# Performance work log

Hardware: AMD Instinct MI355X
Metric: run time of the kernel (lower is better)

The kernel has to match this reference:

```python
import jax, jax.numpy as jnp
import numpy as np
import math

N = 20000          # real nodes (batch_size)
D = 256            # hidden_dim
H = 4              # num_heads
L = 3              # num_layers
E = 320000         # local edges
EXP_DEG = 4        # expander_degree
LN_EPS = 1e-5


def setup_inputs() -> dict:
    key = jax.random.key(0)
    ks = jax.random.split(key, 8)
    x = jax.random.normal(ks[0], (N, D), jnp.float32)
    rng = np.random.default_rng(0)
    edge_index = jnp.asarray(rng.integers(0, N, size=(2, E)), dtype=jnp.int32)
    # Expander: EXP_DEG//2 random permutations on N+1 nodes (incl. virtual node),
    # each contributing edges in both directions -> degree-EXP_DEG regular graph.
    n = N + 1
    perms = [rng.permutation(n) for _ in range(EXP_DEG // 2)]
    src = np.concatenate([np.arange(n) for _ in perms] + perms)
    dst = np.concatenate(perms + [np.arange(n) for _ in perms])
    exp_edge_index = jnp.asarray(np.stack([src, dst]), dtype=jnp.int32)
    s_in = 1.0 / math.sqrt(D)
    s_ffn = 1.0 / math.sqrt(4 * D)
    def w(k, shape, s):
        return jax.random.normal(k, shape, jnp.float32) * s
    params = {
        'Wqkv_loc': w(ks[1], (L, D, 3 * D), s_in), 'bqkv_loc': jnp.zeros((L, 3 * D), jnp.float32),
        'Wo_loc':   w(ks[2], (L, D, D), s_in),     'bo_loc':   jnp.zeros((L, D), jnp.float32),
        'Wqkv_exp': w(ks[3], (L, D, 3 * D), s_in), 'bqkv_exp': jnp.zeros((L, 3 * D), jnp.float32),
        'Wo_exp':   w(ks[4], (L, D, D), s_in),     'bo_exp':   jnp.zeros((L, D), jnp.float32),
        'ln_g': jnp.ones((L, D), jnp.float32),     'ln_b': jnp.zeros((L, D), jnp.float32),
        'W1': w(ks[5], (L, D, 4 * D), s_in),       'b1': jnp.zeros((L, 4 * D), jnp.float32),
        'W2': w(ks[6], (L, 4 * D, D), s_ffn),      'b2': jnp.zeros((L, D), jnp.float32),
    }
    return {'x': x, 'edge_index': edge_index, 'exp_edge_index': exp_edge_index, **params}


def _attention(h, src, dst, Wqkv, bqkv, Wo, bo):
    # Sparse multi-head attention over (src -> dst) edges with segment softmax per dst.
    n, d = h.shape
    dh = d // H
    qkv = (h @ Wqkv + bqkv).reshape(n, 3, H, dh)
    q, k, v = qkv[:, 0], qkv[:, 1], qkv[:, 2]            # [n, H, dh]
    score = (q[dst] * k[src]).sum(-1) / jnp.sqrt(jnp.float32(dh))  # [e, H]
    m = jax.ops.segment_max(score, dst, num_segments=n)  # [n, H]
    ex = jnp.exp(score - m[dst])
    denom = jax.ops.segment_sum(ex, dst, num_segments=n)
    alpha = ex / (denom[dst] + 1e-16)
    out = jax.ops.segment_sum(alpha[:, :, None] * v[src], dst, num_segments=n)  # [n, H, dh]
    return out.reshape(n, d) @ Wo + bo


def _layer_norm(x, g, b):
    mu = x.mean(-1, keepdims=True)
    var = ((x - mu) ** 2).mean(-1, keepdims=True)
    return (x - mu) * jax.lax.rsqrt(var + LN_EPS) * g + b


def reference(x, edge_index, exp_edge_index, Wqkv_loc, bqkv_loc, Wo_loc, bo_loc,
              Wqkv_exp, bqkv_exp, Wo_exp, bo_exp, ln_g, ln_b, W1, b1, W2, b2):
    n0 = x.shape[0]
    # VirtualNode transform: append one zero-feature node connected to/from all nodes.
    h = jnp.concatenate([x, jnp.zeros((1, x.shape[1]), x.dtype)], axis=0)
    ar = jnp.arange(n0, dtype=edge_index.dtype)
    vn = jnp.full((n0,), n0, dtype=edge_index.dtype)
    src = jnp.concatenate([edge_index[0], ar, vn])
    dst = jnp.concatenate([edge_index[1], vn, ar])
    esrc, edst = exp_edge_index[0], exp_edge_index[1]
    for l in range(L):  # fixed small number of structurally distinct layers
        res = h
        loc = _attention(h, src, dst, Wqkv_loc[l], bqkv_loc[l], Wo_loc[l], bo_loc[l])
        exp = _attention(h, esrc, edst, Wqkv_exp[l], bqkv_exp[l], Wo_exp[l], bo_exp[l])
        h = _layer_norm(res + loc + exp, ln_g[l], ln_b[l])
        h = h + (jax.nn.gelu(h @ W1[l] + b1[l], approximate=False) @ W2[l] + b2[l])
    return h[:n0]
```

## Files before the change

### kernel.cpp

```cpp
#include <hip/hip_runtime.h>
#include <stdint.h>

#define NREAL   20000
#define NNODES  20001
#define VN      20000
#define E_EDGES 320000
#define NEXP    80004
#define MPAD    20096
#define NVNW    320

typedef unsigned short u16;
typedef unsigned int   u32;
typedef __bf16 bf16x8 __attribute__((ext_vector_type(8)));
typedef float  f32x4  __attribute__((ext_vector_type(4)));
typedef u16    u16x8  __attribute__((ext_vector_type(8)));

__device__ __host__ __forceinline__ size_t fmoff(int row, int col, int LD) {
    return (size_t)(row >> 4) * ((size_t)LD * 16) + (size_t)((col >> 3) * 128)
         + (size_t)((row & 15) * 8) + (size_t)(col & 7);
}

__device__ __forceinline__ int qkv_perm(int n) {
    if (n < 256) return n;
    int u = n - 256;
    int part = u >> 8;
    int cl = u & 255;
    return 256 + (cl >> 2) * 8 + part * 4 + (cl & 3);
}

__device__ __forceinline__ float bf2f(u16 v) {
    union { u32 u; float f; } x; x.u = ((u32)v) << 16; return x.f;
}
__device__ __forceinline__ u16 f2bf(float f) {
    union { float f; u32 u; } x; x.f = f;
    u32 r = (x.u + 0x7fffu + ((x.u >> 16) & 1u)) >> 16;
    return (u16)r;
}
__device__ __forceinline__ float4 cvt4(ushort4 u) {
    return make_float4(bf2f(u.x), bf2f(u.y), bf2f(u.z), bf2f(u.w));
}
__device__ __forceinline__ float4 ld4bf(const u16* p) { return cvt4(*(const ushort4*)p); }
__device__ __forceinline__ float4 cvtk8(u16x8 r) {
    return make_float4(bf2f(r[0]), bf2f(r[1]), bf2f(r[2]), bf2f(r[3]));
}
__device__ __forceinline__ float4 cvtv8(u16x8 r) {
    return make_float4(bf2f(r[4]), bf2f(r[5]), bf2f(r[6]), bf2f(r[7]));
}


__global__ void hinit_kernel(const float* __restrict__ x, float* __restrict__ h,
                             u16* __restrict__ hb) {
    int idx = blockIdx.x * 256 + threadIdx.x;
    if (idx >= NNODES * 64) return;
    int row = idx >> 6, c0 = (idx & 63) * 4;
    float4 v = make_float4(0.f, 0.f, 0.f, 0.f);
    if (row < NREAL) v = *(const float4*)(x + (size_t)row * 256 + c0);
    *(float4*)(h + (size_t)row * 256 + c0) = v;
    ushort4 o;
    o.x = f2bf(v.x); o.y = f2bf(v.y); o.z = f2bf(v.z); o.w = f2bf(v.w);
    *(ushort4*)(hb + fmoff(row, c0, 256)) = o;
}

__global__ void init_kernel(int* cnt, int* fill, int* ecnt,
                            const float* __restrict__ bl, const float* __restrict__ be,
                            float* __restrict__ bcat,
                            const float* __restrict__ bol, const float* __restrict__ boe,
                            float* __restrict__ bsum) {
    int i = blockIdx.x * 256 + threadIdx.x;
    if (i < NREAL) { cnt[i] = 0; fill[i] = 0; }
    if (i < NNODES) ecnt[i] = 0;
    if (i < 3 * 1536) {
        int l = i / 1536, c = i - l * 1536;
        float v = (c < 768) ? bl[l * 768 + c] : be[l * 768 + c - 768];
        int cc = (c >= 768) ? c - 768 : c;
        int d = qkv_perm(cc) + ((c >= 768) ? 768 : 0);
        bcat[l * 1536 + d] = v;
    }
    if (i < 3 * 256) bsum[i] = bol[i] + boe[i];
}

__global__ void csr_count_kernel(const int* __restrict__ ei, int* __restrict__ cnt) {
    int e = blockIdx.x * 256 + threadIdx.x;
    if (e < E_EDGES) atomicAdd(&cnt[ei[E_EDGES + e]], 1);
}

__global__ void csr_scan_kernel(const int* __restrict__ cnt, int* __restrict__ indptr) {
    __shared__ int ssum[256];
    int t = threadIdx.x;
    int c0 = t * 79;
    int s = 0;
    for (int j = 0; j < 79; j++) {
        int i = c0 + j;
        if (i < NREAL) s += cnt[i];
    }
    ssum[t] = s;
    __syncthreads();
    for (int d2 = 1; d2 < 256; d2 <<= 1) {
        int v = (t >= d2) ? ssum[t - d2] : 0;
        __syncthreads();
        ssum[t] += v;
        __syncthreads();
    }
    int run = (t == 0) ? 0 : ssum[t - 1];
    for (int j = 0; j < 79; j++) {
        int i = c0 + j;
        if (i < NREAL) { indptr[i] = run; run += cnt[i]; }
    }
    if (t == 255) indptr[NREAL] = run;
}

__global__ void csr_scatter_kernel(const int* __restrict__ ei, const int* __restrict__ indptr,
                                   int* __restrict__ fill, int* __restrict__ srcs) {
    int e = blockIdx.x * 256 + threadIdx.x;
    if (e < E_EDGES) {
        int d = ei[E_EDGES + e];
        int pos = indptr[d] + atomicAdd(&fill[d], 1);
        srcs[pos] = ei[e];
    }
}

__global__ void exp_scatter_kernel(const int* __restrict__ eei, int* __restrict__ ecnt,
                                   int* __restrict__ esrcs) {
    int e = blockIdx.x * 256 + threadIdx.x;
    if (e < NEXP) {
        int d = eei[NEXP + e];
        int pos = atomicAdd(&ecnt[d], 1);
        esrcs[d * 4 + pos] = eei[e];
    }
}

__global__ void wconv_all_kernel(const float* __restrict__ WqkvL, const float* __restrict__ WqkvE,
                                 const float* __restrict__ WoL, const float* __restrict__ WoE,
                                 const float* __restrict__ W1, const float* __restrict__ W2,
                                 u16* __restrict__ out) {
    int i = blockIdx.x * 256 + threadIdx.x;
    if (i >= 3 * 1048576) return;
    int l = i / 1048576, r = i - l * 1048576;
    if (r >= 393216 && r < 524288) {
        int r2 = r - 393216;
        int k = r2 >> 8, n = r2 & 255;
        float v = (k < 256) ? WoL[(size_t)l * 65536 + k * 256 + n]
                            : WoE[(size_t)l * 65536 + (k - 256) * 256 + n];
        out[(size_t)l * 1048576 + 393216 + fmoff(n, k, 512)] = f2bf(v);
        return;
    }
    const float* src; int K, N; int base;
    if (r < 196608)      { src = WqkvL; K = 256;  N = 768;  base = 0; }
    else if (r < 393216) { src = WqkvE; K = 256;  N = 768;  base = 196608; }
    else if (r < 786432) { src = W1;    K = 256;  N = 1024; base = 524288; }
    else                 { src = W2;    K = 1024; N = 256;  base = 786432; }
    int r2 = r - base;
    int k = r2 / N, n = r2 - k * N;
    int d = (r < 393216) ? qkv_perm(n) : n;
    out[(size_t)l * 1048576 + base + fmoff(d, k, K)] = f2bf(src[(size_t)l * K * N + r2]);
}

template <int EPI>
__global__ __launch_bounds__(256) void gemm_bn(
    const u16* __restrict__ A, const u16* __restrict__ Bt, const float* __restrict__ bias,
    u16* Cb, u16* Q0, u16* KV0, u16* Q1, u16* KV1, int M, int Nout, int nbn) {
    __shared__ u16 lB[128 * 256];
    const int lin = blockIdx.x;
    const int xcd = lin & 7, rest = lin >> 3;
    const int nt = rest % nbn, mc = xcd + 8 * (rest / nbn);
    const int tn = nt * 128;
    const int tid = threadIdx.x;
    const int w = tid >> 6, lane = tid & 63;
    const int lm = lane & 15, q = lane >> 4;

    {
        const u16* bsrc = Bt + (size_t)(tn >> 4) * 4096;
#pragma unroll
        for (int r = 0; r < 16; r++) {
            int o = (r * 256 + tid) * 8;
            *(bf16x8*)&lB[o] = *(const bf16x8*)&bsrc[o];
        }
    }
    __syncthreads();

    f32x4 acc[2][8];
#pragma unroll
    for (int a = 0; a < 2; a++)
#pragma unroll
        for (int b = 0; b < 8; b++) acc[a][b] = (f32x4)0.0f;

    const int lbo = q * 128 + lm * 8;
    const int maxp = MPAD / 16 - 1;

    bf16x8 aS[3][2], bS[2][8];
#pragma unroll
    for (int s = 0; s < 2; s++) {
        int p0 = (mc * 4) * 8 + w * 2;
#pragma unroll
        for (int f = 0; f < 2; f++) {
            int p = p0 + f; if (p > maxp) p = maxp;
            aS[s][f] = *(const bf16x8*)(A + (size_t)p * 4096 + s * 512 + lbo);
        }
#pragma unroll
        for (int n = 0; n < 8; n++)
            bS[s][n] = *(const bf16x8*)&lB[n * 4096 + s * 512 + lbo];
    }

#pragma unroll
    for (int t = 0; t < 32; t++) {
        const int mt = t >> 3, kk = t & 7;
        if (t + 2 < 32) {
            const int t2 = t + 2, mt2 = t2 >> 3, kk2 = t2 & 7;
            int p0 = (mc * 4 + mt2) * 8 + w * 2;
#pragma unroll
            for (int f = 0; f < 2; f++) {
                int p = p0 + f; if (p > maxp) p = maxp;
                aS[t2 % 3][f] = *(const bf16x8*)(A + (size_t)p * 4096 + kk2 * 512 + lbo);
            }
        }
        if (t >= 1 && t + 1 < 32) {
            const int kk1 = (t + 1) & 7;
#pragma unroll
            for (int n = 0; n < 8; n++)
                bS[(t + 1) & 1][n] = *(const bf16x8*)&lB[n * 4096 + kk1 * 512 + lbo];
        }
#pragma unroll
        for (int mi = 0; mi < 2; mi++)
#pragma unroll
            for (int ni = 0; ni < 8; ni++)
                acc[mi][ni] = __builtin_amdgcn_mfma_f32_16x16x32_bf16(
                    bS[t & 1][ni], aS[t % 3][mi], acc[mi][ni], 0, 0, 0);

        if (kk == 7) {
            const int tmg = (mc * 4 + mt) * 128;
#pragma unroll
            for (int mi = 0; mi < 2; mi++) {
                int grow = tmg + w * 32 + mi * 16 + lm;
                if (grow < M) {
#pragma unroll
                    for (int ni = 0; ni < 8; ni++) {
                        int gcol = tn + ni * 16 + q * 4;
                        float4 b4 = *(const float4*)(bias + gcol);
                        float v0 = acc[mi][ni][0] + b4.x;
                        float v1 = acc[mi][ni][1] + b4.y;
                        float v2 = acc[mi][ni][2] + b4.z;
                        float v3 = acc[mi][ni][3] + b4.w;
                        if constexpr (EPI == 6) {
                            ushort4 o;
                            o.x = f2bf(v0); o.y = f2bf(v1); o.z = f2bf(v2); o.w = f2bf(v3);
                            u16* dst;
                            if (gcol < 256)       dst = Q0  + (size_t)grow * 256 + gcol;
                            else if (gcol < 768)  dst = KV0 + (size_t)grow * 512 + (gcol - 256);
                            else if (gcol < 1024) dst = Q1  + (size_t)grow * 256 + (gcol - 768);
                            else                  dst = KV1 + (size_t)grow * 512 + (gcol - 1024);
                            *(ushort4*)dst = o;
                        } else {
                            float g0, g1, g2, g3;
                            {
                                float u = 0.7978845608f * (v0 + 0.044715f * v0 * v0 * v0);
                                g0 = 0.5f * v0 * (2.0f - 2.0f / (__expf(2.0f * u) + 1.0f));
                            }
                            {
                                float u = 0.7978845608f * (v1 + 0.044715f * v1 * v1 * v1);
                                g1 = 0.5f * v1 * (2.0f - 2.0f / (__expf(2.0f * u) + 1.0f));
                            }
                            {
                                float u = 0.7978845608f * (v2 + 0.044715f * v2 * v2 * v2);
                                g2 = 0.5f * v2 * (2.0f - 2.0f / (__expf(2.0f * u) + 1.0f));
                            }
                            {
                                float u = 0.7978845608f * (v3 + 0.044715f * v3 * v3 * v3);
                                g3 = 0.5f * v3 * (2.0f - 2.0f / (__expf(2.0f * u) + 1.0f));
                            }
                            ushort4 o;
                            o.x = f2bf(g0); o.y = f2bf(g1); o.z = f2bf(g2); o.w = f2bf(g3);
                            *(ushort4*)(Cb + fmoff(grow, gcol, Nout)) = o;
                        }
                    }
                }
#pragma unroll
                for (int ni = 0; ni < 8; ni++) acc[mi][ni] = (f32x4)0.0f;
            }
        }
    }
}

template <int EPI, int K, int MT>
__global__ __launch_bounds__(256) void gemm_fm(
    const u16* __restrict__ A, const u16* __restrict__ Bt, const float* __restrict__ bias,
    u16* Cb, float* Cf, const float* resid, int M, int Nout, int nby) {
    constexpr int MFR = MT / 32;
    constexpr int NK = K / 32;
    const int lin = blockIdx.x;
    const int xcd = lin & 7, sub = lin >> 3;
    const int mtile = xcd + 8 * (sub / nby);
    const int ntile = sub - (sub / nby) * nby;
    const int tm = mtile * MT, tn = ntile * 128;
    if (tm >= M) return;

    const int tid = threadIdx.x;
    const int w = tid >> 6, lane = tid & 63;
    const int lm = lane & 15, q = lane >> 4;
    const int mo = (w >> 1) * (MT / 2), no = (w & 1) * 64;

    f32x4 acc[MFR][4];
#pragma unroll
    for (int a = 0; a < MFR; a++)
#pragma unroll
        for (int b = 0; b < 4; b++) acc[a][b] = (f32x4)0.0f;

    const u16* apf[MFR];
    const u16* bpf[4];
#pragma unroll
    for (int t = 0; t < MFR; t++) {
        int p = (tm + mo) / 16 + t;
        apf[t] = A + (size_t)p * (16 * K) + q * 128 + lm * 8;
    }
#pragma unroll
    for (int n = 0; n < 4; n++) {
        int c = (tn + no) / 16 + n;
        bpf[n] = Bt + (size_t)c * (16 * K) + q * 128 + lm * 8;
    }

    bf16x8 sA[3][MFR], sB[3][4];
#pragma unroll
    for (int s = 0; s < 2 && s < NK; s++) {
#pragma unroll
        for (int t = 0; t < MFR; t++) sA[s][t] = *(const bf16x8*)(apf[t] + s * 512);
#pragma unroll
        for (int n = 0; n < 4; n++) sB[s][n] = *(const bf16x8*)(bpf[n] + s * 512);
    }
#pragma unroll
    for (int i = 0; i < NK; i++) {
        const int cu = i % 3, pf = (i + 2) % 3;
        if (i + 2 < NK) {
#pragma unroll
            for (int t = 0; t < MFR; t++) sA[pf][t] = *(const bf16x8*)(apf[t] + (i + 2) * 512);
#pragma unroll
            for (int n = 0; n < 4; n++) sB[pf][n] = *(const bf16x8*)(bpf[n] + (i + 2) * 512);
        }
#pragma unroll
        for (int mi = 0; mi < MFR; mi++)
#pragma unroll
            for (int ni = 0; ni < 4; ni++)
                acc[mi][ni] = __builtin_amdgcn_mfma_f32_16x16x32_bf16(
                    sB[cu][ni], sA[cu][mi], acc[mi][ni], 0, 0, 0);
    }

    float4 b4[4];
#pragma unroll
    for (int ni = 0; ni < 4; ni++)
        b4[ni] = *(const float4*)(bias + tn + no + ni * 16 + q * 4);

#pragma unroll
    for (int mi = 0; mi < MFR; mi++) {
        int grow = tm + mo + mi * 16 + lm;
        if constexpr (EPI == 4) { if (grow >= NREAL) continue; }
        else                    { if (grow >= M) continue; }
#pragma unroll
        for (int ni = 0; ni < 4; ni++) {
            int gcol = tn + no + ni * 16 + q * 4;
            float v0 = acc[mi][ni][0] + b4[ni].x;
            float v1 = acc[mi][ni][1] + b4[ni].y;
            float v2 = acc[mi][ni][2] + b4[ni].z;
            float v3 = acc[mi][ni][3] + b4[ni].w;
            size_t idx = (size_t)grow * Nout + gcol;
            if constexpr (EPI == 1) {
                *(float4*)(Cf + idx) = make_float4(v0, v1, v2, v3);
            } else if constexpr (EPI == 3) {
                float4 rv = *(const float4*)(resid + idx);
                float o0 = rv.x + v0, o1 = rv.y + v1, o2 = rv.z + v2, o3 = rv.w + v3;
                *(float4*)(Cf + idx) = make_float4(o0, o1, o2, o3);
                ushort4 o;
                o.x = f2bf(o0); o.y = f2bf(o1); o.z = f2bf(o2); o.w = f2bf(o3);
                *(ushort4*)(Cb + fmoff(grow, gcol, Nout)) = o;
            } else {
                float4 rv = *(const float4*)(resid + idx);
                *(float4*)(Cf + idx) = make_float4(rv.x + v0, rv.y + v1, rv.z + v2, rv.w + v3);
            }
        }
    }
}

__global__ void vn_merge_kernel(const float* __restrict__ part, u16* __restrict__ acat) {
    __shared__ float sm[4][64][6];
    int w = threadIdx.x >> 6, lane = threadIdx.x & 63;
    int h = lane >> 4;
    int off = (h << 6) + (lane & 15) * 4;
    float M = -1e30f, L = 0.0f;
    float ax = 0, ay = 0, az = 0, aw = 0;
    for (int p = w * 80; p < w * 80 + 80; p++) {
        const float* pp = part + (size_t)p * 264;
        float pm = pp[h], pl = pp[4 + h];
        float4 nm = *(const float4*)(pp + 8 + off);
        float Mn = fmaxf(M, pm);
        float s0 = __expf(M - Mn);
        float s1 = __expf(pm - Mn);
        ax = ax * s0 + nm.x * s1;
        ay = ay * s0 + nm.y * s1;
        az = az * s0 + nm.z * s1;
        aw = aw * s0 + nm.w * s1;
        L = L * s0 + pl * s1;
        M = Mn;
    }
    sm[w][lane][0] = M; sm[w][lane][1] = L;
    sm[w][lane][2] = ax; sm[w][lane][3] = ay;
    sm[w][lane][4] = az; sm[w][lane][5] = aw;
    __syncthreads();
    if (w == 0) {
        float M2 = -1e30f, L2 = 0.0f;
        float bx = 0, by = 0, bz = 0, bw = 0;
#pragma unroll
        for (int p = 0; p < 4; p++) {
            float pm = sm[p][lane][0], pl = sm[p][lane][1];
            float Mn = fmaxf(M2, pm);
            float s0 = __expf(M2 - Mn);
            float s1 = __expf(pm - Mn);
            bx = bx * s0 + sm[p][lane][2] * s1;
            by = by * s0 + sm[p][lane][3] * s1;
            bz = bz * s0 + sm[p][lane][4] * s1;
            bw = bw * s0 + sm[p][lane][5] * s1;
            L2 = L2 * s0 + pl * s1;
            M2 = Mn;
        }
        float inv = 1.0f / (L2 + 1e-16f);
        ushort4 o;
        o.x = f2bf(bx * inv); o.y = f2bf(by * inv);
        o.z = f2bf(bz * inv); o.w = f2bf(bw * inv);
        *(ushort4*)(acat + fmoff(VN, off, 512)) = o;
    }
}

__global__ void attn_fused_kernel(const u16* __restrict__ qb_loc, const u16* __restrict__ kv_loc,
                                  const u16* __restrict__ qb_exp, const u16* __restrict__ kv_exp,
                                  const int* __restrict__ indptr, const int* __restrict__ srcs,
                                  const int* __restrict__ esrcs,
                                  u16* __restrict__ acat, float* __restrict__ part) {
    int gw0 = (int)((blockIdx.x * (size_t)blockDim.x + threadIdx.x) >> 6);
    int gw = __builtin_amdgcn_readfirstlane(gw0);
    int lane = threadIdx.x & 63;
    int h = lane >> 4;
    int off = (h << 6) + (lane & 15) * 4;
    int coff = (off >> 2) * 8;

    if (gw < NVNW) {
        int wv = gw;
        float4 qv = ld4bf(qb_loc + (size_t)VN * 256 + off);
        float m = -1e30f, l = 0.0f;
        float ax = 0, ay = 0, az = 0, aw = 0;
        for (int i = wv; i < NREAL; i += NVNW) {
            u16x8 r = *(const u16x8*)(kv_loc + (size_t)i * 512 + coff);
            float4 k4 = cvtk8(r);
            float4 v4 = cvtv8(r);
            float s = qv.x * k4.x + qv.y * k4.y + qv.z * k4.z + qv.w * k4.w;
            s += __shfl_xor(s, 1); s += __shfl_xor(s, 2);
            s += __shfl_xor(s, 4); s += __shfl_xor(s, 8);
            float sc = s * 0.125f;
            float mn = fmaxf(m, sc);
            float fold = __expf(m - mn);
            float ee = __expf(sc - mn);
            ax = ax * fold + v4.x * ee;
            ay = ay * fold + v4.y * ee;
            az = az * fold + v4.z * ee;
            aw = aw * fold + v4.w * ee;
            l = l * fold + ee;
            m = mn;
        }
        float* pp = part + (size_t)wv * 264;
        if ((lane & 15) == 0) { pp[h] = m; pp[4 + h] = l; }
        *(float4*)(pp + 8 + off) = make_float4(ax, ay, az, aw);
        return;
    }
    gw -= NVNW;

    const u16 *qb, *kv;
    const int* sl;
    int node, beg, deg, tot, cbase;
    if (gw < NREAL) {
        node = gw; qb = qb_loc; kv = kv_loc; sl = srcs; cbase = 0;
        beg = indptr[node]; deg = indptr[node + 1] - beg; tot = deg + 1;
    } else if (gw < NREAL + NNODES) {
        node = gw - NREAL;
        qb = qb_exp; kv = kv_exp; sl = esrcs; cbase = 256;
        beg = node * 4; deg = 4; tot = 4;
    } else {
        return;
    }

    float4 qv = ld4bf(qb + (size_t)node * 256 + off);
    float m = -1e30f, l = 0.0f;
    float ax = 0, ay = 0, az = 0, aw = 0;

    if (tot <= 4) {
        u16x8 raw[4];
#pragma unroll
        for (int j = 0; j < 4; j++) {
            int s = (j < deg) ? sl[beg + j] : VN;
            raw[j] = *(const u16x8*)(kv + (size_t)s * 512 + coff);
        }
        float sc[4];
#pragma unroll
        for (int j = 0; j < 4; j++) {
            float4 k4 = cvtk8(raw[j]);
            float p = qv.x * k4.x + qv.y * k4.y + qv.z * k4.z + qv.w * k4.w;
            p += __shfl_xor(p, 1); p += __shfl_xor(p, 2);
            p += __shfl_xor(p, 4); p += __shfl_xor(p, 8);
            sc[j] = (j < tot) ? p * 0.125f : -1e30f;
        }
        float mn = fmaxf(fmaxf(sc[0], sc[1]), fmaxf(sc[2], sc[3]));
#pragma unroll
        for (int j = 0; j < 4; j++) {
            float ee = __expf(sc[j] - mn);
            float4 v4 = cvtv8(raw[j]);
            ax += v4.x * ee; ay += v4.y * ee; az += v4.z * ee; aw += v4.w * ee;
            l += ee;
        }
        m = mn;
    } else {
        const int nch = (tot + 7) >> 3;
        u16x8 rA[8], rB[8];
#pragma unroll
        for (int j = 0; j < 8; j++) {
            int s = (j < deg) ? sl[beg + j] : VN;
            rA[j] = *(const u16x8*)(kv + (size_t)s * 512 + coff);
        }
        for (int c = 0; c < nch; c++) {
            if (c + 1 < nch) {
                const int e0n = (c + 1) * 8;
#pragma unroll
                for (int j = 0; j < 8; j++) {
                    int e = e0n + j;
                    int s = (e < deg) ? sl[beg + e] : VN;
                    rB[j] = *(const u16x8*)(kv + (size_t)s * 512 + coff);
                }
            }
            const int e0 = c * 8;
            float sc[8];
#pragma unroll
            for (int j = 0; j < 8; j++) {
                float4 k4 = cvtk8(rA[j]);
                float p = qv.x * k4.x + qv.y * k4.y + qv.z * k4.z + qv.w * k4.w;
                p += __shfl_xor(p, 1); p += __shfl_xor(p, 2);
                p += __shfl_xor(p, 4); p += __shfl_xor(p, 8);
                sc[j] = (e0 + j < tot) ? p * 0.125f : -1e30f;
            }
            float cmax = fmaxf(fmaxf(fmaxf(sc[0], sc[1]), fmaxf(sc[2], sc[3])),
                               fmaxf(fmaxf(sc[4], sc[5]), fmaxf(sc[6], sc[7])));
            float mn = fmaxf(m, cmax);
            float fold = __expf(m - mn);
            ax *= fold; ay *= fold; az *= fold; aw *= fold; l *= fold;
#pragma unroll
            for (int j = 0; j < 8; j++) {
                float ee = __expf(sc[j] - mn);
                float4 v4 = cvtv8(rA[j]);
                ax += v4.x * ee; ay += v4.y * ee; az += v4.z * ee; aw += v4.w * ee;
                l += ee;
            }
            m = mn;
#pragma unroll
            for (int j = 0; j < 8; j++) rA[j] = rB[j];
        }
    }
    float inv = 1.0f / (l + 1e-16f);
    ushort4 o;
    o.x = f2bf(ax * inv); o.y = f2bf(ay * inv);
    o.z = f2bf(az * inv); o.w = f2bf(aw * inv);
    *(ushort4*)(acat + fmoff(node, cbase + off, 512)) = o;
}

__global__ void ln_kernel(const float* hin, const float* __restrict__ asum,
                          const float* __restrict__ g, const float* __restrict__ b,
                          float* hout, u16* __restrict__ hb) {
    int row = blockIdx.x * 4 + (threadIdx.x >> 6);
    if (row >= NNODES) return;
    int lane = threadIdx.x & 63;
    size_t base = (size_t)row * 256 + lane * 4;
    float4 xv = *(const float4*)(hin + base);
    float4 av = *(const float4*)(asum + base);
    xv.x += av.x; xv.y += av.y; xv.z += av.z; xv.w += av.w;
    float s = xv.x + xv.y + xv.z + xv.w;
#pragma unroll
    for (int o = 1; o < 64; o <<= 1) s += __shfl_xor(s, o);
    float mu = s * (1.0f / 256.0f);
    float dx = xv.x - mu, dy = xv.y - mu, dz = xv.z - mu, dw = xv.w - mu;
    float ss = dx * dx + dy * dy + dz * dz + dw * dw;
#pragma unroll
    for (int o = 1; o < 64; o <<= 1) ss += __shfl_xor(ss, o);
    float var = ss * (1.0f / 256.0f);
    float inv = 1.0f / sqrtf(var + 1e-5f);
    float4 gv = *(const float4*)(g + lane * 4);
    float4 bv = *(const float4*)(b + lane * 4);
    float4 y;
    y.x = dx * inv * gv.x + bv.x;
    y.y = dy * inv * gv.y + bv.y;
    y.z = dz * inv * gv.z + bv.z;
    y.w = dw * inv * gv.w + bv.w;
    *(float4*)(hout + base) = y;
    ushort4 o4;
    o4.x = f2bf(y.x); o4.y = f2bf(y.y); o4.z = f2bf(y.z); o4.w = f2bf(y.w);
    *(ushort4*)(hb + fmoff(row, lane * 4, 256)) = o4;
}


extern "C" void kernel_launch(void* const* d_in, const int* in_sizes, int n_in,
                              void* d_out, int out_size, void* d_ws, size_t ws_size,
                              hipStream_t stream) {
    (void)in_sizes; (void)n_in; (void)out_size; (void)ws_size;
    const float* x        = (const float*)d_in[0];
    const int*   ei       = (const int*)d_in[1];
    const int*   eei      = (const int*)d_in[2];
    const float* Wqkv_loc = (const float*)d_in[3];
    const float* bqkv_loc = (const float*)d_in[4];
    const float* Wo_loc   = (const float*)d_in[5];
    const float* bo_loc   = (const float*)d_in[6];
    const float* Wqkv_exp = (const float*)d_in[7];
    const float* bqkv_exp = (const float*)d_in[8];
    const float* Wo_exp   = (const float*)d_in[9];
    const float* bo_exp   = (const float*)d_in[10];
    const float* ln_g     = (const float*)d_in[11];
    const float* ln_b     = (const float*)d_in[12];
    const float* W1       = (const float*)d_in[13];
    const float* b1       = (const float*)d_in[14];
    const float* W2       = (const float*)d_in[15];
    const float* b2       = (const float*)d_in[16];

    char* wsp = (char*)d_ws;
    size_t off = 0;
    auto carve = [&](size_t bytes) -> void* {
        void* p = wsp + off;
        off += (bytes + 255) & ~(size_t)255;
        return p;
    };
    float* h_f    = (float*)carve((size_t)NNODES * 256 * 4);
    u16*   h_b    = (u16*)carve((size_t)MPAD * 256 * 2);
    u16*   qb_loc = (u16*)carve((size_t)NNODES * 256 * 2);
    u16*   kv_loc = (u16*)carve((size_t)NNODES * 512 * 2);
    u16*   qb_exp = (u16*)carve((size_t)NNODES * 256 * 2);
    u16*   kv_exp = (u16*)carve((size_t)NNODES * 512 * 2);
    u16*   acat   = (u16*)carve((size_t)MPAD * 512 * 2);
    float* asum   = (float*)carve((size_t)NNODES * 256 * 4);
    u16*   wbf    = (u16*)carve((size_t)3 * 1048576 * 2);
    float* bcat   = (float*)carve((size_t)3 * 1536 * 4);
    float* bsum   = (float*)carve((size_t)3 * 256 * 4);
    int*   cnt    = (int*)carve((size_t)NREAL * 4);
    int*   indptr = (int*)carve((size_t)(NREAL + 1) * 4);
    int*   fill   = (int*)carve((size_t)NREAL * 4);
    int*   srcs   = (int*)carve((size_t)E_EDGES * 4);
    int*   ecnt   = (int*)carve((size_t)NNODES * 4);
    int*   esrcs  = (int*)carve((size_t)NNODES * 4 * 4);
    float* part   = (float*)carve((size_t)NVNW * 264 * 4);
    u16*   mid    = qb_loc;

    hinit_kernel<<<(NNODES * 64 + 255) / 256, 256, 0, stream>>>(x, h_f, h_b);
    init_kernel<<<(NNODES + 255) / 256, 256, 0, stream>>>(
        cnt, fill, ecnt, bqkv_loc, bqkv_exp, bcat, bo_loc, bo_exp, bsum);
    csr_count_kernel<<<(E_EDGES + 255) / 256, 256, 0, stream>>>(ei, cnt);
    csr_scan_kernel<<<1, 256, 0, stream>>>(cnt, indptr);
    csr_scatter_kernel<<<(E_EDGES + 255) / 256, 256, 0, stream>>>(ei, indptr, fill, srcs);
    exp_scatter_kernel<<<(NEXP + 255) / 256, 256, 0, stream>>>(eei, ecnt, esrcs);
    wconv_all_kernel<<<(3 * 1048576 + 255) / 256, 256, 0, stream>>>(
        Wqkv_loc, Wqkv_exp, Wo_loc, Wo_exp, W1, W2, wbf);

    const int NBM64 = 320;
    const int ATTN_BLOCKS = (NVNW + NREAL + NNODES + 3) / 4;

    for (int l = 0; l < 3; l++) {
        const u16* wqkvC = wbf + (size_t)l * 1048576 + 0;
        const u16* wocat = wbf + (size_t)l * 1048576 + 393216;
        const u16* w1T   = wbf + (size_t)l * 1048576 + 524288;
        const u16* w2T   = wbf + (size_t)l * 1048576 + 786432;

        gemm_bn<6><<<480, 256, 0, stream>>>(
            h_b, wqkvC, bcat + l * 1536, nullptr,
            qb_loc, kv_loc, qb_exp, kv_exp, NNODES, 1536, 12);

        attn_fused_kernel<<<ATTN_BLOCKS, 256, 0, stream>>>(
            qb_loc, kv_loc, qb_exp, kv_exp, indptr, srcs, esrcs, acat, part);
        vn_merge_kernel<<<1, 256, 0, stream>>>(part, acat);

        gemm_fm<1, 512, 64><<<NBM64 * 2, 256, 0, stream>>>(
            acat, wocat, bsum + l * 256, nullptr, asum, nullptr, NNODES, 256, 2);

        ln_kernel<<<(NNODES + 3) / 4, 256, 0, stream>>>(
            h_f, asum, ln_g + l * 256, ln_b + l * 256, h_f, h_b);

        gemm_bn<2><<<320, 256, 0, stream>>>(
            h_b, w1T, b1 + l * 1024, mid,
            nullptr, nullptr, nullptr, nullptr, NNODES, 1024, 8);
        if (l < 2) {
            gemm_fm<3, 1024, 64><<<NBM64 * 2, 256, 0, stream>>>(
                mid, w2T, b2 + l * 256, h_b, h_f, h_f, NNODES, 256, 2);
        } else {
            gemm_fm<4, 1024, 64><<<NBM64 * 2, 256, 0, stream>>>(
                mid, w2T, b2 + l * 256, nullptr, (float*)d_out, h_f, NNODES, 256, 2);
        }
    }
}
```

Before: 816.5 us.

## Fuse residual add and LayerNorm into full-row output-projection GEMM epilogue

Replaces the 64x128-tile output GEMM with a full-row 64x256 tile kernel, so each block owns entire rows. That lets the attention output projection do the residual add and LayerNorm in its epilogue through a small shared-memory reduction, which removes the separate ln_kernel launch and the fp32 asum round trip to memory. The FFN down-projection also uses the full-row tile, which halves the block count (320 blocks) and may lower occupancy and parallelism across CUs. One risk is that rows at or beyond M still read the residual in the epilogue before the bounds check.

```diff
diff --git a/kernel.cpp b/kernel.cpp
--- a/kernel.cpp
+++ b/kernel.cpp
@@ -280,62 +280,56 @@
     }
 }
 
-template <int EPI, int K, int MT>
-__global__ __launch_bounds__(256) void gemm_fm(
+template <int EPI, int K>
+__global__ __launch_bounds__(256) void gemm_rw(
     const u16* __restrict__ A, const u16* __restrict__ Bt, const float* __restrict__ bias,
-    u16* Cb, float* Cf, const float* resid, int M, int Nout, int nby) {
-    constexpr int MFR = MT / 32;
+    u16* __restrict__ Cb, float* __restrict__ Cf, const float* __restrict__ resid,
+    const float* __restrict__ g, const float* __restrict__ bvec, int M) {
     constexpr int NK = K / 32;
+    __shared__ float smS[64][4];
+    __shared__ float smQ[64][4];
     const int lin = blockIdx.x;
-    const int xcd = lin & 7, sub = lin >> 3;
-    const int mtile = xcd + 8 * (sub / nby);
-    const int ntile = sub - (sub / nby) * nby;
-    const int tm = mtile * MT, tn = ntile * 128;
+    const int mtile = (lin & 7) + 8 * (lin >> 3);
+    const int tm = mtile * 64;
     if (tm >= M) return;
-
     const int tid = threadIdx.x;
     const int w = tid >> 6, lane = tid & 63;
     const int lm = lane & 15, q = lane >> 4;
-    const int mo = (w >> 1) * (MT / 2), no = (w & 1) * 64;
-
-    f32x4 acc[MFR][4];
-#pragma unroll
-    for (int a = 0; a < MFR; a++)
+
+    f32x4 acc[4][4];
+#pragma unroll
+    for (int a = 0; a < 4; a++)
 #pragma unroll
         for (int b = 0; b < 4; b++) acc[a][b] = (f32x4)0.0f;
 
-    const u16* apf[MFR];
+    const u16* apf[4];
     const u16* bpf[4];
 #pragma unroll
-    for (int t = 0; t < MFR; t++) {
-        int p = (tm + mo) / 16 + t;
-        apf[t] = A + (size_t)p * (16 * K) + q * 128 + lm * 8;
-    }
-#pragma unroll
-    for (int n = 0; n < 4; n++) {
-        int c = (tn + no) / 16 + n;
-        bpf[n] = Bt + (size_t)c * (16 * K) + q * 128 + lm * 8;
-    }
-
-    bf16x8 sA[3][MFR], sB[3][4];
+    for (int mi = 0; mi < 4; mi++)
+        apf[mi] = A + (size_t)(tm / 16 + mi) * (16 * K) + q * 128 + lm * 8;
+#pragma unroll
+    for (int ni = 0; ni < 4; ni++)
+        bpf[ni] = Bt + (size_t)(w * 4 + ni) * (16 * K) + q * 128 + lm * 8;
+
+    bf16x8 sA[3][4], sB[3][4];
 #pragma unroll
     for (int s = 0; s < 2 && s < NK; s++) {
 #pragma unroll
-        for (int t = 0; t < MFR; t++) sA[s][t] = *(const bf16x8*)(apf[t] + s * 512);
-#pragma unroll
-        for (int n = 0; n < 4; n++) sB[s][n] = *(const bf16x8*)(bpf[n] + s * 512);
+        for (int mi = 0; mi < 4; mi++) sA[s][mi] = *(const bf16x8*)(apf[mi] + s * 512);
+#pragma unroll
+        for (int ni = 0; ni < 4; ni++) sB[s][ni] = *(const bf16x8*)(bpf[ni] + s * 512);
     }
 #pragma unroll
     for (int i = 0; i < NK; i++) {
         const int cu = i % 3, pf = (i + 2) % 3;
         if (i + 2 < NK) {
 #pragma unroll
-            for (int t = 0; t < MFR; t++) sA[pf][t] = *(const bf16x8*)(apf[t] + (i + 2) * 512);
-#pragma unroll
-            for (int n = 0; n < 4; n++) sB[pf][n] = *(const bf16x8*)(bpf[n] + (i + 2) * 512);
-        }
-#pragma unroll
-        for (int mi = 0; mi < MFR; mi++)
+            for (int mi = 0; mi < 4; mi++) sA[pf][mi] = *(const bf16x8*)(apf[mi] + (i + 2) * 512);
+#pragma unroll
+            for (int ni = 0; ni < 4; ni++) sB[pf][ni] = *(const bf16x8*)(bpf[ni] + (i + 2) * 512);
+        }
+#pragma unroll
+        for (int mi = 0; mi < 4; mi++)
 #pragma unroll
             for (int ni = 0; ni < 4; ni++)
                 acc[mi][ni] = __builtin_amdgcn_mfma_f32_16x16x32_bf16(
@@ -345,33 +339,108 @@
     float4 b4[4];
 #pragma unroll
     for (int ni = 0; ni < 4; ni++)
-        b4[ni] = *(const float4*)(bias + tn + no + ni * 16 + q * 4);
-
-#pragma unroll
-    for (int mi = 0; mi < MFR; mi++) {
-        int grow = tm + mo + mi * 16 + lm;
-        if constexpr (EPI == 4) { if (grow >= NREAL) continue; }
-        else                    { if (grow >= M) continue; }
+        b4[ni] = *(const float4*)(bias + w * 64 + ni * 16 + q * 4);
+#pragma unroll
+    for (int mi = 0; mi < 4; mi++) {
+        int grow = tm + mi * 16 + lm;
 #pragma unroll
         for (int ni = 0; ni < 4; ni++) {
-            int gcol = tn + no + ni * 16 + q * 4;
-            float v0 = acc[mi][ni][0] + b4[ni].x;
-            float v1 = acc[mi][ni][1] + b4[ni].y;
-            float v2 = acc[mi][ni][2] + b4[ni].z;
-            float v3 = acc[mi][ni][3] + b4[ni].w;
-            size_t idx = (size_t)grow * Nout + gcol;
-            if constexpr (EPI == 1) {
-                *(float4*)(Cf + idx) = make_float4(v0, v1, v2, v3);
-            } else if constexpr (EPI == 3) {
-                float4 rv = *(const float4*)(resid + idx);
-                float o0 = rv.x + v0, o1 = rv.y + v1, o2 = rv.z + v2, o3 = rv.w + v3;
-                *(float4*)(Cf + idx) = make_float4(o0, o1, o2, o3);
+            int gcol = w * 64 + ni * 16 + q * 4;
+            size_t idx = (size_t)grow * 256 + gcol;
+            float4 rv = *(const float4*)(resid + idx);
+            acc[mi][ni][0] = rv.x + (acc[mi][ni][0] + b4[ni].x);
+            acc[mi][ni][1] = rv.y + (acc[mi][ni][1] + b4[ni].y);
+            acc[mi][ni][2] = rv.z + (acc[mi][ni][2] + b4[ni].z);
+            acc[mi][ni][3] = rv.w + (acc[mi][ni][3] + b4[ni].w);
+        }
+    }
+
+    if constexpr (EPI == 5) {
+        float s1[4];
+#pragma unroll
+        for (int mi = 0; mi < 4; mi++) {
+            float s = 0.f;
+#pragma unroll
+            for (int ni = 0; ni < 4; ni++)
+                s += acc[mi][ni][0] + acc[mi][ni][1] + acc[mi][ni][2] + acc[mi][ni][3];
+            s += __shfl_xor(s, 16); s += __shfl_xor(s, 32);
+            s1[mi] = s;
+        }
+        if (lane < 16) {
+#pragma unroll
+            for (int mi = 0; mi < 4; mi++) smS[mi * 16 + lm][w] = s1[mi];
+        }
+        __syncthreads();
+        float mu[4];
+#pragma unroll
+        for (int mi = 0; mi < 4; mi++) {
+            int r = mi * 16 + lm;
+            mu[mi] = (smS[r][0] + smS[r][1] + smS[r][2] + smS[r][3]) * (1.0f / 256.0f);
+        }
+        float s2[4];
+#pragma unroll
+        for (int mi = 0; mi < 4; mi++) {
+            float s = 0.f;
+#pragma unroll
+            for (int ni = 0; ni < 4; ni++) {
+                float d0 = acc[mi][ni][0] - mu[mi];
+                float d1 = acc[mi][ni][1] - mu[mi];
+                float d2 = acc[mi][ni][2] - mu[mi];
+                float d3 = acc[mi][ni][3] - mu[mi];
+                s += d0 * d0 + d1 * d1 + d2 * d2 + d3 * d3;
+            }
+            s += __shfl_xor(s, 16); s += __shfl_xor(s, 32);
+            s2[mi] = s;
+        }
+        if (lane < 16) {
+#pragma unroll
+            for (int mi = 0; mi < 4; mi++) smQ[mi * 16 + lm][w] = s2[mi];
+        }
+        __syncthreads();
+        float rinv[4];
+#pragma unroll
+        for (int mi = 0; mi < 4; mi++) {
+            int r = mi * 16 + lm;
+            float var = (smQ[r][0] + smQ[r][1] + smQ[r][2] + smQ[r][3]) * (1.0f / 256.0f);
+            rinv[mi] = 1.0f / sqrtf(var + 1e-5f);
+        }
+#pragma unroll
+        for (int mi = 0; mi < 4; mi++) {
+            int grow = tm + mi * 16 + lm;
+            if (grow >= M) continue;
+#pragma unroll
+            for (int ni = 0; ni < 4; ni++) {
+                int gcol = w * 64 + ni * 16 + q * 4;
+                float4 gv = *(const float4*)(g + gcol);
+                float4 bv = *(const float4*)(bvec + gcol);
+                float4 y;
+                y.x = (acc[mi][ni][0] - mu[mi]) * rinv[mi] * gv.x + bv.x;
+                y.y = (acc[mi][ni][1] - mu[mi]) * rinv[mi] * gv.y + bv.y;
+                y.z = (acc[mi][ni][2] - mu[mi]) * rinv[mi] * gv.z + bv.z;
+                y.w = (acc[mi][ni][3] - mu[mi]) * rinv[mi] * gv.w + bv.w;
+                *(float4*)(Cf + (size_t)grow * 256 + gcol) = y;
                 ushort4 o;
-                o.x = f2bf(o0); o.y = f2bf(o1); o.z = f2bf(o2); o.w = f2bf(o3);
-                *(ushort4*)(Cb + fmoff(grow, gcol, Nout)) = o;
-            } else {
-                float4 rv = *(const float4*)(resid + idx);
-                *(float4*)(Cf + idx) = make_float4(rv.x + v0, rv.y + v1, rv.z + v2, rv.w + v3);
+                o.x = f2bf(y.x); o.y = f2bf(y.y); o.z = f2bf(y.z); o.w = f2bf(y.w);
+                *(ushort4*)(Cb + fmoff(grow, gcol, 256)) = o;
+            }
+        }
+    } else {
+#pragma unroll
+        for (int mi = 0; mi < 4; mi++) {
+            int grow = tm + mi * 16 + lm;
+            if constexpr (EPI == 4) { if (grow >= NREAL) continue; }
+            else                    { if (grow >= M) continue; }
+#pragma unroll
+            for (int ni = 0; ni < 4; ni++) {
+                int gcol = w * 64 + ni * 16 + q * 4;
+                *(float4*)(Cf + (size_t)grow * 256 + gcol) =
+                    make_float4(acc[mi][ni][0], acc[mi][ni][1], acc[mi][ni][2], acc[mi][ni][3]);
+                if constexpr (EPI == 3) {
+                    ushort4 o;
+                    o.x = f2bf(acc[mi][ni][0]); o.y = f2bf(acc[mi][ni][1]);
+                    o.z = f2bf(acc[mi][ni][2]); o.w = f2bf(acc[mi][ni][3]);
+                    *(ushort4*)(Cb + fmoff(grow, gcol, 256)) = o;
+                }
             }
         }
     }
@@ -563,39 +632,6 @@
     *(ushort4*)(acat + fmoff(node, cbase + off, 512)) = o;
 }
 
-__global__ void ln_kernel(const float* hin, const float* __restrict__ asum,
-                          const float* __restrict__ g, const float* __restrict__ b,
-                          float* hout, u16* __restrict__ hb) {
-    int row = blockIdx.x * 4 + (threadIdx.x >> 6);
-    if (row >= NNODES) return;
-    int lane = threadIdx.x & 63;
-    size_t base = (size_t)row * 256 + lane * 4;
-    float4 xv = *(const float4*)(hin + base);
-    float4 av = *(const float4*)(asum + base);
-    xv.x += av.x; xv.y += av.y; xv.z += av.z; xv.w += av.w;
-    float s = xv.x + xv.y + xv.z + xv.w;
-#pragma unroll
-    for (int o = 1; o < 64; o <<= 1) s += __shfl_xor(s, o);
-    float mu = s * (1.0f / 256.0f);
-    float dx = xv.x - mu, dy = xv.y - mu, dz = xv.z - mu, dw = xv.w - mu;
-    float ss = dx * dx + dy * dy + dz * dz + dw * dw;
-#pragma unroll
-    for (int o = 1; o < 64; o <<= 1) ss += __shfl_xor(ss, o);
-    float var = ss * (1.0f / 256.0f);
-    float inv = 1.0f / sqrtf(var + 1e-5f);
-    float4 gv = *(const float4*)(g + lane * 4);
-    float4 bv = *(const float4*)(b + lane * 4);
-    float4 y;
-    y.x = dx * inv * gv.x + bv.x;
-    y.y = dy * inv * gv.y + bv.y;
-    y.z = dz * inv * gv.z + bv.z;
-    y.w = dw * inv * gv.w + bv.w;
-    *(float4*)(hout + base) = y;
-    ushort4 o4;
-    o4.x = f2bf(y.x); o4.y = f2bf(y.y); o4.z = f2bf(y.z); o4.w = f2bf(y.w);
-    *(ushort4*)(hb + fmoff(row, lane * 4, 256)) = o4;
-}
-
 
 extern "C" void kernel_launch(void* const* d_in, const int* in_sizes, int n_in,
                               void* d_out, int out_size, void* d_ws, size_t ws_size,
@@ -633,7 +669,6 @@
     u16*   qb_exp = (u16*)carve((size_t)NNODES * 256 * 2);
     u16*   kv_exp = (u16*)carve((size_t)NNODES * 512 * 2);
     u16*   acat   = (u16*)carve((size_t)MPAD * 512 * 2);
-    float* asum   = (float*)carve((size_t)NNODES * 256 * 4);
     u16*   wbf    = (u16*)carve((size_t)3 * 1048576 * 2);
     float* bcat   = (float*)carve((size_t)3 * 1536 * 4);
     float* bsum   = (float*)carve((size_t)3 * 256 * 4);
@@ -656,8 +691,8 @@
     wconv_all_kernel<<<(3 * 1048576 + 255) / 256, 256, 0, stream>>>(
         Wqkv_loc, Wqkv_exp, Wo_loc, Wo_exp, W1, W2, wbf);
 
-    const int NBM64 = 320;
     const int ATTN_BLOCKS = (NVNW + NREAL + NNODES + 3) / 4;
+    const int NB64 = 320;
 
     for (int l = 0; l < 3; l++) {
         const u16* wqkvC = wbf + (size_t)l * 1048576 + 0;
@@ -673,21 +708,20 @@
             qb_loc, kv_loc, qb_exp, kv_exp, indptr, srcs, esrcs, acat, part);
         vn_merge_kernel<<<1, 256, 0, stream>>>(part, acat);
 
-        gemm_fm<1, 512, 64><<<NBM64 * 2, 256, 0, stream>>>(
-            acat, wocat, bsum + l * 256, nullptr, asum, nullptr, NNODES, 256, 2);
-
-        ln_kernel<<<(NNODES + 3) / 4, 256, 0, stream>>>(
-            h_f, asum, ln_g + l * 256, ln_b + l * 256, h_f, h_b);
+        gemm_rw<5, 512><<<NB64, 256, 0, stream>>>(
+            acat, wocat, bsum + l * 256, h_b, h_f, h_f,
+            ln_g + l * 256, ln_b + l * 256, NNODES);
 
         gemm_bn<2><<<320, 256, 0, stream>>>(
             h_b, w1T, b1 + l * 1024, mid,
             nullptr, nullptr, nullptr, nullptr, NNODES, 1024, 8);
+
         if (l < 2) {
-            gemm_fm<3, 1024, 64><<<NBM64 * 2, 256, 0, stream>>>(
-                mid, w2T, b2 + l * 256, h_b, h_f, h_f, NNODES, 256, 2);
+            gemm_rw<3, 1024><<<NB64, 256, 0, stream>>>(
+                mid, w2T, b2 + l * 256, h_b, h_f, h_f, nullptr, nullptr, NNODES);
         } else {
-            gemm_fm<4, 1024, 64><<<NBM64 * 2, 256, 0, stream>>>(
-                mid, w2T, b2 + l * 256, nullptr, (float*)d_out, h_f, NNODES, 256, 2);
-        }
-    }
-}
+            gemm_rw<4, 1024><<<NB64, 256, 0, stream>>>(
+                mid, w2T, b2 + l * 256, nullptr, (float*)d_out, h_f, nullptr, nullptr, NNODES);
+        }
+    }
+}
```

New measurement: 1.112 ms. 36.2% more time.

## Replace FFN1 GEMM with register-direct MFMA kernel and dedicated mid buffer

Applied to the files above, without the earlier changes.

Adds a dedicated FFN first-layer kernel in which each block computes a 64x256 tile and loads A and B fragments directly from global memory into registers with a three-stage software prefetch, instead of using the shared-memory gemm_bn path. GELU is fused into its epilogue, and the gemm_bn epilogue is reduced to the QKV-only path. The FFN intermediate now gets its own workspace buffer when the workspace is large enough, rather than aliasing the Q buffer. The aim is to cut LDS traffic and synchronisation and to raise block count for better occupancy. The cost is that the A tile is reloaded once per N-slice and there is no LDS reuse across waves.

```diff
diff --git a/kernel.cpp b/kernel.cpp
--- a/kernel.cpp
+++ b/kernel.cpp
@@ -240,42 +240,110 @@
                         float v1 = acc[mi][ni][1] + b4.y;
                         float v2 = acc[mi][ni][2] + b4.z;
                         float v3 = acc[mi][ni][3] + b4.w;
-                        if constexpr (EPI == 6) {
-                            ushort4 o;
-                            o.x = f2bf(v0); o.y = f2bf(v1); o.z = f2bf(v2); o.w = f2bf(v3);
-                            u16* dst;
-                            if (gcol < 256)       dst = Q0  + (size_t)grow * 256 + gcol;
-                            else if (gcol < 768)  dst = KV0 + (size_t)grow * 512 + (gcol - 256);
-                            else if (gcol < 1024) dst = Q1  + (size_t)grow * 256 + (gcol - 768);
-                            else                  dst = KV1 + (size_t)grow * 512 + (gcol - 1024);
-                            *(ushort4*)dst = o;
-                        } else {
-                            float g0, g1, g2, g3;
-                            {
-                                float u = 0.7978845608f * (v0 + 0.044715f * v0 * v0 * v0);
-                                g0 = 0.5f * v0 * (2.0f - 2.0f / (__expf(2.0f * u) + 1.0f));
-                            }
-                            {
-                                float u = 0.7978845608f * (v1 + 0.044715f * v1 * v1 * v1);
-                                g1 = 0.5f * v1 * (2.0f - 2.0f / (__expf(2.0f * u) + 1.0f));
-                            }
-                            {
-                                float u = 0.7978845608f * (v2 + 0.044715f * v2 * v2 * v2);
-                                g2 = 0.5f * v2 * (2.0f - 2.0f / (__expf(2.0f * u) + 1.0f));
-                            }
-                            {
-                                float u = 0.7978845608f * (v3 + 0.044715f * v3 * v3 * v3);
-                                g3 = 0.5f * v3 * (2.0f - 2.0f / (__expf(2.0f * u) + 1.0f));
-                            }
-                            ushort4 o;
-                            o.x = f2bf(g0); o.y = f2bf(g1); o.z = f2bf(g2); o.w = f2bf(g3);
-                            *(ushort4*)(Cb + fmoff(grow, gcol, Nout)) = o;
-                        }
+                        ushort4 o;
+                        o.x = f2bf(v0); o.y = f2bf(v1); o.z = f2bf(v2); o.w = f2bf(v3);
+                        u16* dst;
+                        if (gcol < 256)       dst = Q0  + (size_t)grow * 256 + gcol;
+                        else if (gcol < 768)  dst = KV0 + (size_t)grow * 512 + (gcol - 256);
+                        else if (gcol < 1024) dst = Q1  + (size_t)grow * 256 + (gcol - 768);
+                        else                  dst = KV1 + (size_t)grow * 512 + (gcol - 1024);
+                        *(ushort4*)dst = o;
                     }
                 }
 #pragma unroll
                 for (int ni = 0; ni < 8; ni++) acc[mi][ni] = (f32x4)0.0f;
             }
+        }
+    }
+}
+
+__global__ __launch_bounds__(256) void ffn1_rw(
+    const u16* __restrict__ A, const u16* __restrict__ Bt, const float* __restrict__ bias,
+    u16* __restrict__ Cb, int M) {
+    const int lin = blockIdx.x;
+    const int mt = lin >> 2, ns = lin & 3;
+    const int tm = mt * 64;
+    if (tm >= M) return;
+    const int tid = threadIdx.x;
+    const int w = tid >> 6, lane = tid & 63;
+    const int lm = lane & 15, q = lane >> 4;
+
+    f32x4 acc[4][4];
+#pragma unroll
+    for (int a = 0; a < 4; a++)
+#pragma unroll
+        for (int b = 0; b < 4; b++) acc[a][b] = (f32x4)0.0f;
+
+    const u16* apf[4];
+    const u16* bpf[4];
+#pragma unroll
+    for (int mi = 0; mi < 4; mi++)
+        apf[mi] = A + (size_t)(tm / 16 + mi) * 4096 + q * 128 + lm * 8;
+#pragma unroll
+    for (int ni = 0; ni < 4; ni++)
+        bpf[ni] = Bt + (size_t)(ns * 16 + w * 4 + ni) * 4096 + q * 128 + lm * 8;
+
+    bf16x8 sA[3][4], sB[3][4];
+#pragma unroll
+    for (int s = 0; s < 2; s++) {
+#pragma unroll
+        for (int mi = 0; mi < 4; mi++) sA[s][mi] = *(const bf16x8*)(apf[mi] + s * 512);
+#pragma unroll
+        for (int ni = 0; ni < 4; ni++) sB[s][ni] = *(const bf16x8*)(bpf[ni] + s * 512);
+    }
+#pragma unroll
+    for (int i = 0; i < 8; i++) {
+        const int cu = i % 3, pf = (i + 2) % 3;
+        if (i + 2 < 8) {
+#pragma unroll
+            for (int mi = 0; mi < 4; mi++) sA[pf][mi] = *(const bf16x8*)(apf[mi] + (i + 2) * 512);
+#pragma unroll
+            for (int ni = 0; ni < 4; ni++) sB[pf][ni] = *(const bf16x8*)(bpf[ni] + (i + 2) * 512);
+        }
+#pragma unroll
+        for (int mi = 0; mi < 4; mi++)
+#pragma unroll
+            for (int ni = 0; ni < 4; ni++)
+                acc[mi][ni] = __builtin_amdgcn_mfma_f32_16x16x32_bf16(
+                    sB[cu][ni], sA[cu][mi], acc[mi][ni], 0, 0, 0);
+    }
+
+    float4 b4[4];
+#pragma unroll
+    for (int ni = 0; ni < 4; ni++)
+        b4[ni] = *(const float4*)(bias + ns * 256 + w * 64 + ni * 16 + q * 4);
+
+#pragma unroll
+    for (int mi = 0; mi < 4; mi++) {
+        int grow = tm + mi * 16 + lm;
+        if (grow >= M) continue;
+#pragma unroll
+        for (int ni = 0; ni < 4; ni++) {
+            int gcol = ns * 256 + w * 64 + ni * 16 + q * 4;
+            float v0 = acc[mi][ni][0] + b4[ni].x;
+            float v1 = acc[mi][ni][1] + b4[ni].y;
+            float v2 = acc[mi][ni][2] + b4[ni].z;
+            float v3 = acc[mi][ni][3] + b4[ni].w;
+            float g0, g1, g2, g3;
+            {
+                float u = 0.7978845608f * (v0 + 0.044715f * v0 * v0 * v0);
+                g0 = 0.5f * v0 * (2.0f - 2.0f / (__expf(2.0f * u) + 1.0f));
+            }
+            {
+                float u = 0.7978845608f * (v1 + 0.044715f * v1 * v1 * v1);
+                g1 = 0.5f * v1 * (2.0f - 2.0f / (__expf(2.0f * u) + 1.0f));
+            }
+            {
+                float u = 0.7978845608f * (v2 + 0.044715f * v2 * v2 * v2);
+                g2 = 0.5f * v2 * (2.0f - 2.0f / (__expf(2.0f * u) + 1.0f));
+            }
+            {
+                float u = 0.7978845608f * (v3 + 0.044715f * v3 * v3 * v3);
+                g3 = 0.5f * v3 * (2.0f - 2.0f / (__expf(2.0f * u) + 1.0f));
+            }
+            ushort4 o;
+            o.x = f2bf(g0); o.y = f2bf(g1); o.z = f2bf(g2); o.w = f2bf(g3);
+            *(ushort4*)(Cb + fmoff(grow, gcol, 1024)) = o;
         }
     }
 }
@@ -600,7 +668,7 @@
 extern "C" void kernel_launch(void* const* d_in, const int* in_sizes, int n_in,
                               void* d_out, int out_size, void* d_ws, size_t ws_size,
                               hipStream_t stream) {
-    (void)in_sizes; (void)n_in; (void)out_size; (void)ws_size;
+    (void)in_sizes; (void)n_in; (void)out_size;
     const float* x        = (const float*)d_in[0];
     const int*   ei       = (const int*)d_in[1];
     const int*   eei      = (const int*)d_in[2];
@@ -644,7 +712,8 @@
     int*   ecnt   = (int*)carve((size_t)NNODES * 4);
     int*   esrcs  = (int*)carve((size_t)NNODES * 4 * 4);
     float* part   = (float*)carve((size_t)NVNW * 264 * 4);
-    u16*   mid    = qb_loc;
+    u16*   mid_d  = (u16*)carve((size_t)MPAD * 1024 * 2);
+    u16*   mid    = (ws_size >= off) ? mid_d : qb_loc;
 
     hinit_kernel<<<(NNODES * 64 + 255) / 256, 256, 0, stream>>>(x, h_f, h_b);
     init_kernel<<<(NNODES + 255) / 256, 256, 0, stream>>>(
@@ -679,9 +748,9 @@
         ln_kernel<<<(NNODES + 3) / 4, 256, 0, stream>>>(
             h_f, asum, ln_g + l * 256, ln_b + l * 256, h_f, h_b);
 
-        gemm_bn<2><<<320, 256, 0, stream>>>(
-            h_b, w1T, b1 + l * 1024, mid,
-            nullptr, nullptr, nullptr, nullptr, NNODES, 1024, 8);
+        ffn1_rw<<<320 * 4, 256, 0, stream>>>(
+            h_b, w1T, b1 + l * 1024, mid, NNODES);
+
         if (l < 2) {
             gemm_fm<3, 1024, 64><<<NBM64 * 2, 256, 0, stream>>>(
                 mid, w2T, b2 + l * 256, h_b, h_f, h_f, NNODES, 256, 2);
```

New measurement: 798.2 us. 2.2% less time.
